# Kernel tuning notes

Hardware: AMD Instinct MI355X
Metric: run time of the kernel (lower is better)

## Reference

```python
import jax, jax.numpy as jnp
import numpy as np

B, P, ENC, DEC, ATT, EMB, V, T = 128, 196, 2048, 512, 512, 512, 10000, 30


def setup_inputs() -> dict:
    key = jax.random.key(0)
    ks = jax.random.split(key, 16)

    def lin(k, o, i, s=0.02):
        k1, k2 = jax.random.split(k)
        return (jax.random.normal(k1, (o, i), jnp.float32) * s,
                jax.random.normal(k2, (o,), jnp.float32) * s)

    enc_out = jax.random.normal(ks[0], (B, P, ENC), jnp.float32)
    enc_caps = jax.random.randint(ks[1], (B, T), 0, V)
    len_caps = jax.random.randint(ks[2], (B, 1), 2, T + 1)  # lengths in [2, T]

    W_enc_att, b_enc_att = lin(ks[3], ATT, ENC)
    W_dec_att, b_dec_att = lin(ks[4], ATT, DEC)
    W_att, b_att = lin(ks[5], 1, ATT)
    W_init_h, b_init_h = lin(ks[6], DEC, ENC)
    W_init_c, b_init_c = lin(ks[7], DEC, ENC)
    W_ih, b_ih = lin(ks[8], 4 * DEC, EMB + ENC)
    W_hh, b_hh = lin(ks[9], 4 * DEC, DEC)
    W_fbeta, b_fbeta = lin(ks[10], ENC, DEC)
    emb = jax.random.uniform(ks[11], (V, EMB), jnp.float32, -0.1, 0.1)
    W_fc = jax.random.uniform(ks[12], (V, DEC), jnp.float32, -0.1, 0.1)
    b_fc = jnp.zeros((V,), jnp.float32)

    return dict(enc_out=enc_out, enc_caps=enc_caps, len_caps=len_caps, emb=emb,
                W_enc_att=W_enc_att, b_enc_att=b_enc_att,
                W_dec_att=W_dec_att, b_dec_att=b_dec_att,
                W_att=W_att, b_att=b_att,
                W_init_h=W_init_h, b_init_h=b_init_h,
                W_init_c=W_init_c, b_init_c=b_init_c,
                W_ih=W_ih, b_ih=b_ih, W_hh=W_hh, b_hh=b_hh,
                W_fbeta=W_fbeta, b_fbeta=b_fbeta,
                W_fc=W_fc, b_fc=b_fc)


def _forward(enc_out, enc_caps, len_caps, emb,
             W_enc_att, b_enc_att, W_dec_att, b_dec_att, W_att, b_att,
             W_init_h, b_init_h, W_init_c, b_init_c,
             W_ih, b_ih, W_hh, b_hh, W_fbeta, b_fbeta, W_fc, b_fc):
    lens = len_caps[:, 0]
    order = jnp.argsort(-lens)  # sort descending by caption length
    lens = lens[order]
    caps = enc_caps[order]
    enc = enc_out[order]  # [B,P,ENC]
    len_dec = lens - 1
    Tm = caps.shape[1] - 1  # static upper bound on decode steps; masked per row

    embeds = emb[caps[:, :Tm]]  # [B,Tm,EMB]
    mu = enc.mean(axis=1)
    h = mu @ W_init_h.T + b_init_h
    c = mu @ W_init_c.T + b_init_c
    att_enc = enc @ W_enc_att.T + b_enc_att  # [B,P,ATT], invariant over t

    def step(carry, inp):
        h, c = carry
        t, emb_t = inp
        att_dec = h @ W_dec_att.T + b_dec_att  # [B,ATT]
        e = (jax.nn.relu(att_enc + att_dec[:, None, :]) @ W_att.T + b_att)[..., 0]  # [B,P]
        alpha = jax.nn.softmax(e, axis=1)
        weighted = jnp.einsum('bpd,bp->bd', enc, alpha)  # [B,ENC]
        gate = jax.nn.sigmoid(h @ W_fbeta.T + b_fbeta)
        x = jnp.concatenate([emb_t, weighted * gate], axis=1)  # [B,EMB+ENC]
        gates = x @ W_ih.T + b_ih + h @ W_hh.T + b_hh
        i, f, g, o = jnp.split(gates, 4, axis=1)  # torch LSTMCell gate order
        c_new = jax.nn.sigmoid(f) * c + jax.nn.sigmoid(i) * jnp.tanh(g)
        h_new = jax.nn.sigmoid(o) * jnp.tanh(c_new)
        preds = h_new @ W_fc.T + b_fc  # dropout is identity at eval
        m = (t < len_dec).astype(h.dtype)[:, None]  # shrinking-batch mask
        h = m * h_new + (1 - m) * h
        c = m * c_new + (1 - m) * c
        return (h, c), (preds * m, alpha * m)

    ts = jnp.arange(Tm)
    (_, _), (preds, alphas) = jax.lax.scan(step, (h, c), (ts, jnp.swapaxes(embeds, 0, 1)))
    predictions = jnp.swapaxes(preds, 0, 1)  # [B,Tm,V]
    alphas = jnp.swapaxes(alphas, 0, 1)      # [B,Tm,P]
    return caps, len_dec, predictions, alphas, order


def reference(enc_out, enc_caps, len_caps, emb,
              W_enc_att, b_enc_att, W_dec_att, b_dec_att, W_att, b_att,
              W_init_h, b_init_h, W_init_c, b_init_c,
              W_ih, b_ih, W_hh, b_hh, W_fbeta, b_fbeta, W_fc, b_fc):
    return _forward(enc_out, enc_caps, len_caps, emb,
                    W_enc_att, b_enc_att, W_dec_att, b_dec_att, W_att, b_att,
                    W_init_h, b_init_h, W_init_c, b_init_c,
                    W_ih, b_ih, W_hh, b_hh, W_fbeta, b_fbeta, W_fc, b_fc)
```

## Files before the change

### kernel.cpp

```cpp
#include <hip/hip_runtime.h>
#include <hip/hip_bf16.h>
#include <math.h>

#define NB   128
#define NP   196
#define DENC 2048
#define DDEC 512
#define NV   10000
#define NT   30
#define NTM  29

typedef __attribute__((ext_vector_type(8))) short short8;
typedef __attribute__((ext_vector_type(4))) float f32x4;

__device__ __forceinline__ float sigmoidf_(float x) { return 1.f / (1.f + __expf(-x)); }
__device__ __forceinline__ unsigned short f2bf(float x) {
    unsigned int u = __float_as_uint(x);
    u += 0x7fffu + ((u >> 16) & 1u);
    return (unsigned short)(u >> 16);
}
__device__ __forceinline__ float bf2f(unsigned short h) {
    return __uint_as_float(((unsigned int)h) << 16);
}

__global__ void sort_kernel(const int* __restrict__ len_caps,
                            const int* __restrict__ enc_caps,
                            float* __restrict__ out_caps,
                            float* __restrict__ out_lendec,
                            float* __restrict__ out_order,
                            int* __restrict__ order_ws,
                            int* __restrict__ nt_ws,
                            int* __restrict__ caps_ws) {
    __shared__ int lens[NB];
    int i = threadIdx.x;
    lens[i] = len_caps[i];
    __syncthreads();
    int li = lens[i];
    int r = 0;
    for (int j = 0; j < NB; ++j) {
        int lj = lens[j];
        if (lj > li || (lj == li && j < i)) r++;
    }
    order_ws[r]   = i;
    out_order[r]  = (float)i;
    out_lendec[r] = (float)(li - 1);
    for (int k = 0; k < NT; ++k) {
        int cv = enc_caps[i * NT + k];
        caps_ws[r * NT + k]  = cv;
        out_caps[r * NT + k] = (float)cv;
    }
    if (i < NTM) {
        int cnt = 0;
        for (int j = 0; j < NB; ++j) cnt += (lens[j] - 1 > i) ? 1 : 0;
        nt_ws[i] = cnt;
    }
}

__global__ void rowmap_kernel(const int* __restrict__ order, int* __restrict__ rowmap) {
    int m = blockIdx.x * 256 + threadIdx.x;
    rowmap[m] = order[m / NP] * NP + (m % NP);
}

__global__ void mu_kernel(const float* __restrict__ enc,
                          const int* __restrict__ order,
                          float* __restrict__ mu) {
    int b = blockIdx.x;
    int d = blockIdx.y * 256 + threadIdx.x;
    const float* eb = enc + (long)order[b] * NP * DENC;
    float s = 0.f;
    for (int p = 0; p < NP; ++p) s += eb[(long)p * DENC + d];
    mu[(long)b * DENC + d] = s * (1.f / (float)NP);
}

__global__ void fill_zero4(float4* __restrict__ p, int n4) {
    int i = blockIdx.x * 256 + threadIdx.x;
    if (i < n4) p[i] = make_float4(0.f, 0.f, 0.f, 0.f);
}

__global__ void conv_bf(const float* __restrict__ s, unsigned short* __restrict__ d, int n) {
    int i = blockIdx.x * 256 + threadIdx.x;
    if (i < n) d[i] = f2bf(s[i]);
}

__global__ void kconcat_ihh(const float* __restrict__ W_ih, const float* __restrict__ W_hh,
                            unsigned short* __restrict__ dst) {
    int n = blockIdx.y;
    int k = blockIdx.x * 256 + threadIdx.x;
    float v = (k < 2560) ? W_ih[(long)n * 2560 + k] : W_hh[(long)n * 512 + (k - 2560)];
    dst[(long)n * 3072 + k] = f2bf(v);
}

__global__ void bias_add2(const float* __restrict__ a, const float* __restrict__ b,
                          float* __restrict__ d, int n) {
    int i = blockIdx.x * 256 + threadIdx.x;
    if (i < n) d[i] = a[i] + b[i];
}

__global__ __launch_bounds__(256) void gemm_mfma(
    const float* __restrict__ A, long lda, const int* __restrict__ rowmap,
    const unsigned short* __restrict__ W, long ldw,
    const float* __restrict__ bias0, const float* __restrict__ bias1, int split,
    float* __restrict__ out0, long ld0, float* __restrict__ out1, long ld1,
    unsigned short* __restrict__ outbf,
    int act0, int act1, int M, int N, int K,
    const int* __restrict__ nt, int t, long zstride, int abf) {
    __shared__ __align__(16) unsigned short As[64 * 32];
    __shared__ __align__(16) unsigned short Bs[128 * 32];
    const int limit = nt ? nt[t] : M;

    int bx = blockIdx.x, by = blockIdx.y;
    if (!nt) {
        int nwg = gridDim.x * gridDim.y;
        int lin = by * gridDim.x + bx;
        int q = nwg >> 3, r = nwg & 7;
        int xcd = lin & 7, i = lin >> 3;
        int sw = (xcd < r ? xcd * (q + 1) : r * (q + 1) + (xcd - r) * q) + i;
        bx = sw % gridDim.x;
        by = sw / gridDim.x;
    }

    const int m0 = by * 64;
    if (m0 >= limit) return;
    const int n0 = bx * 128;
    const int tid = threadIdx.x;
    const int kz = blockIdx.z * K;

    const int arow = tid >> 2, akc = tid & 3;
    const int aws = (akc ^ ((arow >> 1) & 3)) * 8;
    const int brow = tid >> 1, bkc = (tid & 1) * 2;
    const int bss = (brow >> 1) & 3;
    const int bws0 = (bkc ^ bss) * 8;
    const int bws1 = ((bkc + 1) ^ bss) * 8;

    long aRowG = m0 + arow;
    if (rowmap) aRowG = rowmap[aRowG];
    const float* aptrf = nullptr;
    const unsigned short* aptrh = nullptr;
    if (abf) aptrh = (const unsigned short*)A + aRowG * lda + akc * 8 + kz;
    else     aptrf = A + aRowG * lda + akc * 8 + kz;
    const int gnw = n0 + brow;
    const bool wvalid = gnw < N;
    const unsigned short* wptr = W + (long)(wvalid ? gnw : 0) * ldw + bkc * 8 + kz;

    if (blockIdx.z) out0 += (long)blockIdx.z * zstride;

    const int lane = tid & 63, wv = tid >> 6;
    const int wm = wv & 1, wn = wv >> 1;
    const int fcol = lane & 15, quad = lane >> 4;
    const int sx = (fcol >> 1) & 3;
    const unsigned short* aFp = As + ((wm * 32 + fcol) * 32 + ((quad ^ sx) * 8));
    const unsigned short* bFp = Bs + ((wn * 64 + fcol) * 32 + ((quad ^ sx) * 8));

    f32x4 acc[2][4];
#pragma unroll
    for (int i = 0; i < 2; ++i)
#pragma unroll
        for (int j = 0; j < 4; ++j) acc[i][j] = (f32x4){0.f, 0.f, 0.f, 0.f};

    for (int k0 = 0; k0 < K; k0 += 32) {
        short8 ap;
        if (abf) {
            ap = *(const short8*)(aptrh);
            aptrh += 32;
        } else {
            float4 x0 = *(const float4*)(aptrf);
            float4 x1 = *(const float4*)(aptrf + 4);
            aptrf += 32;
            ap[0] = (short)f2bf(x0.x); ap[1] = (short)f2bf(x0.y);
            ap[2] = (short)f2bf(x0.z); ap[3] = (short)f2bf(x0.w);
            ap[4] = (short)f2bf(x1.x); ap[5] = (short)f2bf(x1.y);
            ap[6] = (short)f2bf(x1.z); ap[7] = (short)f2bf(x1.w);
        }
        int4 w0 = make_int4(0, 0, 0, 0), w1 = w0;
        if (wvalid) {
            w0 = *(const int4*)(wptr);
            w1 = *(const int4*)(wptr + 8);
        }
        wptr += 32;
        __syncthreads();
        *(short8*)(As + (arow * 32 + aws)) = ap;
        *(int4*)(Bs + (brow * 32 + bws0)) = w0;
        *(int4*)(Bs + (brow * 32 + bws1)) = w1;
        __syncthreads();
        short8 a0 = *(const short8*)(aFp);
        short8 a1 = *(const short8*)(aFp + 512);
#pragma unroll
        for (int ns = 0; ns < 4; ++ns) {
            short8 bn = *(const short8*)(bFp + ns * 512);
            acc[0][ns] = __builtin_amdgcn_mfma_f32_16x16x32_bf16(a0, bn, acc[0][ns], 0, 0, 0);
            acc[1][ns] = __builtin_amdgcn_mfma_f32_16x16x32_bf16(a1, bn, acc[1][ns], 0, 0, 0);
        }
    }

#pragma unroll
    for (int ms = 0; ms < 2; ++ms) {
        int gmb = m0 + wm * 32 + ms * 16 + quad * 4;
#pragma unroll
        for (int ns = 0; ns < 4; ++ns) {
            int gn = n0 + wn * 64 + ns * 16 + fcol;
            if (gn >= N) continue;
            int seg = (gn >= split);
            float bv = seg ? (bias1 ? bias1[gn - split] : 0.f)
                           : (bias0 ? bias0[gn] : 0.f);
            int act = seg ? act1 : act0;
#pragma unroll
            for (int r = 0; r < 4; ++r) {
                int gm = gmb + r;
                if (gm >= limit) continue;
                float v = acc[ms][ns][r] + bv;
                if (act == 1) v = sigmoidf_(v);
                if (outbf && !seg) outbf[(long)gm * ld0 + gn] = f2bf(v);
                else if (!seg) out0[(long)gm * ld0 + gn] = v;
                else out1[(long)gm * ld1 + (gn - split)] = v;
            }
        }
    }
}

__global__ __launch_bounds__(256) void alpha_kernel(
    const unsigned short* __restrict__ att_enc,
    const float* __restrict__ adg,
    const float* __restrict__ W_att, const float* __restrict__ b_att,
    const float* __restrict__ emb, const int* __restrict__ caps,
    const unsigned short* __restrict__ h_bf,
    const int* __restrict__ nt,
    float* __restrict__ al_g,
    float* __restrict__ out_alpha,
    unsigned short* __restrict__ xh, int t) {
    int b = blockIdx.x;
    if (b >= nt[t]) return;
    int tid = threadIdx.x, lane = tid & 63, wid = tid >> 6;
    __shared__ float es[NP];
    __shared__ float stats[2];

    const float* adp = adg + (long)b * 2560 + lane * 8;
    float4 ad0 = *(const float4*)(adp);
    float4 ad1 = *(const float4*)(adp + 4);
    const float* wap = W_att + lane * 8;
    float4 wa0 = *(const float4*)(wap);
    float4 wa1 = *(const float4*)(wap + 4);
    float ad[8] = {ad0.x, ad0.y, ad0.z, ad0.w, ad1.x, ad1.y, ad1.z, ad1.w};
    float wa[8] = {wa0.x, wa0.y, wa0.z, wa0.w, wa1.x, wa1.y, wa1.z, wa1.w};
    float batt = b_att[0];

    for (int p = wid; p < NP; p += 4) {
        const unsigned short* row = att_enc + ((long)b * NP + p) * 512 + lane * 8;
        int4 rv = *(const int4*)row;
        const unsigned short* us = (const unsigned short*)&rv;
        float s = 0.f;
#pragma unroll
        for (int j = 0; j < 8; ++j) {
            float v = bf2f(us[j]) + ad[j];
            v = v > 0.f ? v : 0.f;
            s += v * wa[j];
        }
#pragma unroll
        for (int o = 32; o; o >>= 1) s += __shfl_xor(s, o, 64);
        if (lane == 0) es[p] = s + batt;
    }
    __syncthreads();
    if (wid == 0) {
        float v[4], mx = -1e30f;
#pragma unroll
        for (int i = 0; i < 4; ++i) {
            int p = lane + 64 * i;
            v[i] = (p < NP) ? es[p] : -1e30f;
            mx = fmaxf(mx, v[i]);
        }
#pragma unroll
        for (int o = 32; o; o >>= 1) mx = fmaxf(mx, __shfl_xor(mx, o, 64));
        float s = 0.f;
#pragma unroll
        for (int i = 0; i < 4; ++i) {
            int p = lane + 64 * i;
            if (p < NP) s += __expf(v[i] - mx);
        }
#pragma unroll
        for (int o = 32; o; o >>= 1) s += __shfl_xor(s, o, 64);
        if (lane == 0) { stats[0] = mx; stats[1] = 1.f / s; }
    }
    __syncthreads();
    float mm = stats[0], inv = stats[1];
    if (tid < NP) {
        float a = __expf(es[tid] - mm) * inv;
        al_g[(long)b * NP + tid] = a;
        out_alpha[((long)b * NTM + t) * NP + tid] = a;
    }
    int cap = caps[b * NT + t];
    float2 ev = *(const float2*)(emb + (long)cap * 512 + tid * 2);
    unsigned int pk = (unsigned int)f2bf(ev.x) | ((unsigned int)f2bf(ev.y) << 16);
    *(unsigned int*)(xh + (long)b * 3072 + tid * 2) = pk;
    unsigned int hv = *(const unsigned int*)(h_bf + (long)b * DDEC + tid * 2);
    *(unsigned int*)(xh + (long)b * 3072 + 2560 + tid * 2) = hv;
}

__global__ __launch_bounds__(256) void wx_kernel(
    const float* __restrict__ al_g,
    const float* __restrict__ adg,
    const float* __restrict__ enc, const int* __restrict__ order,
    const int* __restrict__ nt,
    unsigned short* __restrict__ xh, int t) {
    int b = blockIdx.x;
    if (b >= nt[t]) return;
    int d = blockIdx.y * 256 + threadIdx.x;
    __shared__ float al[NP];
    if (threadIdx.x < NP) al[threadIdx.x] = al_g[(long)b * NP + threadIdx.x];
    __syncthreads();
    const float* eb = enc + ((long)order[b] * NP) * DENC + d;
    float acc = 0.f;
#pragma unroll 4
    for (int p = 0; p < NP; ++p) acc += al[p] * eb[(long)p * DENC];
    float gate = adg[(long)b * 2560 + 512 + d];
    xh[(long)b * 3072 + 512 + d] = f2bf(acc * gate);
}

__global__ void lstm_kernel(const float* __restrict__ gp,
                            const float* __restrict__ bihh,
                            float* __restrict__ c,
                            unsigned short* __restrict__ h_bf,
                            const int* __restrict__ nt, int t) {
    int b = blockIdx.y;
    if (b >= nt[t]) return;
    int d = blockIdx.x * 256 + threadIdx.x;
    const long S = (long)NB * 2048;
    const float* g = gp + ((long)b << 11);
    float ig = sigmoidf_(g[d]        + g[S + d]        + g[2*S + d]        + bihh[d]);
    float fg = sigmoidf_(g[512 + d]  + g[S + 512 + d]  + g[2*S + 512 + d]  + bihh[512 + d]);
    float gg = tanhf(    g[1024 + d] + g[S + 1024 + d] + g[2*S + 1024 + d] + bihh[1024 + d]);
    float og = sigmoidf_(g[1536 + d] + g[S + 1536 + d] + g[2*S + 1536 + d] + bihh[1536 + d]);
    long idx = (long)b * DDEC + d;
    float cn = fg * c[idx] + ig * gg;
    c[idx] = cn;
    h_bf[idx] = f2bf(og * tanhf(cn));
}

extern "C" void kernel_launch(void* const* d_in, const int* in_sizes, int n_in,
                              void* d_out, int out_size, void* d_ws, size_t ws_size,
                              hipStream_t stream) {
    const float* enc_out   = (const float*)d_in[0];
    const int*   enc_caps  = (const int*)d_in[1];
    const int*   len_caps  = (const int*)d_in[2];
    const float* emb       = (const float*)d_in[3];
    const float* W_enc_att = (const float*)d_in[4];
    const float* b_enc_att = (const float*)d_in[5];
    const float* W_dec_att = (const float*)d_in[6];
    const float* b_dec_att = (const float*)d_in[7];
    const float* W_att     = (const float*)d_in[8];
    const float* b_att     = (const float*)d_in[9];
    const float* W_init_h  = (const float*)d_in[10];
    const float* b_init_h  = (const float*)d_in[11];
    const float* W_init_c  = (const float*)d_in[12];
    const float* b_init_c  = (const float*)d_in[13];
    const float* W_ih      = (const float*)d_in[14];
    const float* b_ih      = (const float*)d_in[15];
    const float* W_hh      = (const float*)d_in[16];
    const float* b_hh      = (const float*)d_in[17];
    const float* W_fbeta   = (const float*)d_in[18];
    const float* b_fbeta   = (const float*)d_in[19];
    const float* W_fc      = (const float*)d_in[20];
    const float* b_fc      = (const float*)d_in[21];

    float* out        = (float*)d_out;
    float* out_caps   = out;
    float* out_lendec = out + 3840;
    float* out_pred   = out + 3968;
    float* out_alpha  = out + 3968 + 37120000;
    float* out_order  = out + 3968 + 37120000 + 727552;

    char*  wsb = (char*)d_ws;
    size_t off = 0;
    auto alloc = [&](size_t bytes) -> void* {
        void* p = wsb + off;
        off += (bytes + 255) & ~(size_t)255;
        return p;
    };
    int*   order_ws = (int*)alloc(NB * 4);
    int*   nt_ws    = (int*)alloc(NTM * 4);
    int*   caps_ws  = (int*)alloc(NB * NT * 4);
    int*   rowmap   = (int*)alloc((size_t)NB * NP * 4);
    float* mu       = (float*)alloc((size_t)NB * DENC * 4);
    float* c        = (float*)alloc((size_t)NB * DDEC * 4);
    float* adg      = (float*)alloc((size_t)NB * 2560 * 4);
    float* al_g     = (float*)alloc((size_t)NB * NP * 4);
    float* gates    = (float*)alloc((size_t)3 * NB * 2048 * 4);
    unsigned short* h_bf = (unsigned short*)alloc((size_t)NB * DDEC * 2);
    unsigned short* xh   = (unsigned short*)alloc((size_t)NB * 3072 * 2);
    unsigned short* att_enc_bf = (unsigned short*)alloc((size_t)NB * NP * 512 * 2);
    unsigned short* Wq_enc  = (unsigned short*)alloc((size_t)512 * 2048 * 2);
    unsigned short* Wq_init = (unsigned short*)alloc((size_t)1024 * 2048 * 2);
    unsigned short* Wq_adg  = (unsigned short*)alloc((size_t)2560 * 512 * 2);
    unsigned short* Wq_ihh  = (unsigned short*)alloc((size_t)2048 * 3072 * 2);
    unsigned short* Wq_fc   = (unsigned short*)alloc((size_t)NV * 512 * 2);
    float* bihh = (float*)alloc(2048 * 4);

    sort_kernel<<<1, NB, 0, stream>>>(len_caps, enc_caps, out_caps, out_lendec,
                                      out_order, order_ws, nt_ws, caps_ws);
    fill_zero4<<<36960, 256, 0, stream>>>((float4*)out_pred, 9461888);
    rowmap_kernel<<<98, 256, 0, stream>>>(order_ws, rowmap);
    mu_kernel<<<dim3(NB, DENC / 256), 256, 0, stream>>>(enc_out, order_ws, mu);

    conv_bf<<<(512 * 2048) / 256, 256, 0, stream>>>(W_enc_att, Wq_enc, 512 * 2048);
    conv_bf<<<(512 * 2048) / 256, 256, 0, stream>>>(W_init_h, Wq_init, 512 * 2048);
    conv_bf<<<(512 * 2048) / 256, 256, 0, stream>>>(W_init_c, Wq_init + (size_t)512 * 2048, 512 * 2048);
    conv_bf<<<(512 * 512) / 256, 256, 0, stream>>>(W_dec_att, Wq_adg, 512 * 512);
    conv_bf<<<(2048 * 512) / 256, 256, 0, stream>>>(W_fbeta, Wq_adg + (size_t)512 * 512, 2048 * 512);
    kconcat_ihh<<<dim3(12, 2048), 256, 0, stream>>>(W_ih, W_hh, Wq_ihh);
    conv_bf<<<(NV * 512) / 256, 256, 0, stream>>>(W_fc, Wq_fc, NV * 512);
    bias_add2<<<8, 256, 0, stream>>>(b_ih, b_hh, bihh, 2048);

    gemm_mfma<<<dim3(8, 2), 256, 0, stream>>>(
        mu, DENC, nullptr, Wq_init, DENC,
        b_init_h, b_init_c, 512,
        nullptr, DDEC, c, DDEC, h_bf, 0, 0,
        NB, 1024, DENC, nullptr, 0, 0, 0);

    gemm_mfma<<<dim3(4, 392), 256, 0, stream>>>(
        enc_out, DENC, rowmap, Wq_enc, DENC,
        b_enc_att, nullptr, 512,
        nullptr, 512, nullptr, 0, att_enc_bf, 0, 0,
        NB * NP, 512, DENC, nullptr, 0, 0, 0);

    for (int t = 0; t < NTM; ++t) {
        gemm_mfma<<<dim3(20, 2), 256, 0, stream>>>(
            (const float*)h_bf, DDEC, nullptr, Wq_adg, DDEC,
            b_dec_att, b_fbeta, 512,
            adg, 2560, adg + 512, 2560, nullptr, 0, 1,
            NB, 2560, DDEC, nt_ws, t, 0, 1);
        alpha_kernel<<<NB, 256, 0, stream>>>(
            att_enc_bf, adg, W_att, b_att, emb, caps_ws, h_bf, nt_ws,
            al_g, out_alpha, xh, t);
        wx_kernel<<<dim3(NB, 8), 256, 0, stream>>>(
            al_g, adg, enc_out, order_ws, nt_ws, xh, t);
        gemm_mfma<<<dim3(16, 2, 3), 256, 0, stream>>>(
            (const float*)xh, 3072, nullptr, Wq_ihh, 3072,
            nullptr, nullptr, 2048,
            gates, 2048, nullptr, 0, nullptr, 0, 0,
            NB, 2048, 1024, nt_ws, t, (long)NB * 2048, 1);
        lstm_kernel<<<dim3(2, NB), 256, 0, stream>>>(gates, bihh, c, h_bf, nt_ws, t);
        gemm_mfma<<<dim3(79, 2), 256, 0, stream>>>(
            (const float*)h_bf, DDEC, nullptr, Wq_fc, DDEC,
            b_fc, nullptr, NV,
            out_pred + (long)t * NV, (long)NTM * NV, nullptr, 0, nullptr, 0, 0,
            NB, NV, DDEC, nt_ws, t, 0, 1);
    }
}
```

Baseline: 4.086 ms.

## Pre-convert sorted encoder output to bf16 and double-buffer GEMM LDS tiles

Adds a kernel that gathers the encoder output in sorted order and converts it to bf16 once. The mean, attention-encoder GEMM and the per-step weighted-context kernel then read this half-size copy instead of the fp32 tensor, which cuts the bandwidth of the 29 repeated wx passes. The GEMM also gets double-buffered shared memory with a register prefetch, so global loads overlap the MFMA work and one barrier per k-step is removed. The cost is an extra 100 MB buffer and one conversion pass, and the mean and context sums are now taken over bf16-rounded inputs, which loses some precision.

```diff
diff --git a/kernel.cpp b/kernel.cpp
--- a/kernel.cpp
+++ b/kernel.cpp
@@ -61,15 +61,34 @@
     rowmap[m] = order[m / NP] * NP + (m % NP);
 }
 
-__global__ void mu_kernel(const float* __restrict__ enc,
-                          const int* __restrict__ order,
+__global__ void conv_enc_bf(const float* __restrict__ enc, const int* __restrict__ rowmap,
+                            unsigned short* __restrict__ dst) {
+    long m = blockIdx.x;
+    int d = threadIdx.x * 8;
+    const float* src = enc + (long)rowmap[m] * DENC + d;
+    float4 x0 = *(const float4*)(src);
+    float4 x1 = *(const float4*)(src + 4);
+    short8 v;
+    v[0] = (short)f2bf(x0.x); v[1] = (short)f2bf(x0.y);
+    v[2] = (short)f2bf(x0.z); v[3] = (short)f2bf(x0.w);
+    v[4] = (short)f2bf(x1.x); v[5] = (short)f2bf(x1.y);
+    v[6] = (short)f2bf(x1.z); v[7] = (short)f2bf(x1.w);
+    *(short8*)(dst + m * DENC + d) = v;
+}
+
+__global__ void mu_kernel(const unsigned short* __restrict__ enc_bfs,
                           float* __restrict__ mu) {
     int b = blockIdx.x;
-    int d = blockIdx.y * 256 + threadIdx.x;
-    const float* eb = enc + (long)order[b] * NP * DENC;
-    float s = 0.f;
-    for (int p = 0; p < NP; ++p) s += eb[(long)p * DENC + d];
-    mu[(long)b * DENC + d] = s * (1.f / (float)NP);
+    int d = (blockIdx.y * 256 + threadIdx.x) * 2;
+    const unsigned short* eb = enc_bfs + (long)b * NP * DENC + d;
+    float s0 = 0.f, s1 = 0.f;
+    for (int p = 0; p < NP; ++p) {
+        unsigned int pk = *(const unsigned int*)(eb + (long)p * DENC);
+        s0 += bf2f((unsigned short)(pk & 0xffffu));
+        s1 += bf2f((unsigned short)(pk >> 16));
+    }
+    mu[(long)b * DENC + d]     = s0 * (1.f / (float)NP);
+    mu[(long)b * DENC + d + 1] = s1 * (1.f / (float)NP);
 }
 
 __global__ void fill_zero4(float4* __restrict__ p, int n4) {
@@ -104,8 +123,8 @@
     unsigned short* __restrict__ outbf,
     int act0, int act1, int M, int N, int K,
     const int* __restrict__ nt, int t, long zstride, int abf) {
-    __shared__ __align__(16) unsigned short As[64 * 32];
-    __shared__ __align__(16) unsigned short Bs[128 * 32];
+    __shared__ __align__(16) unsigned short As[2][64 * 32];
+    __shared__ __align__(16) unsigned short Bs[2][128 * 32];
     const int limit = nt ? nt[t] : M;
 
     int bx = blockIdx.x, by = blockIdx.y;
@@ -148,8 +167,8 @@
     const int wm = wv & 1, wn = wv >> 1;
     const int fcol = lane & 15, quad = lane >> 4;
     const int sx = (fcol >> 1) & 3;
-    const unsigned short* aFp = As + ((wm * 32 + fcol) * 32 + ((quad ^ sx) * 8));
-    const unsigned short* bFp = Bs + ((wn * 64 + fcol) * 32 + ((quad ^ sx) * 8));
+    const int aOff = (wm * 32 + fcol) * 32 + ((quad ^ sx) * 8);
+    const int bOff = (wn * 64 + fcol) * 32 + ((quad ^ sx) * 8);
 
     f32x4 acc[2][4];
 #pragma unroll
@@ -157,39 +176,60 @@
 #pragma unroll
         for (int j = 0; j < 4; ++j) acc[i][j] = (f32x4){0.f, 0.f, 0.f, 0.f};
 
-    for (int k0 = 0; k0 < K; k0 += 32) {
-        short8 ap;
-        if (abf) {
-            ap = *(const short8*)(aptrh);
-            aptrh += 32;
-        } else {
-            float4 x0 = *(const float4*)(aptrf);
-            float4 x1 = *(const float4*)(aptrf + 4);
-            aptrf += 32;
-            ap[0] = (short)f2bf(x0.x); ap[1] = (short)f2bf(x0.y);
-            ap[2] = (short)f2bf(x0.z); ap[3] = (short)f2bf(x0.w);
-            ap[4] = (short)f2bf(x1.x); ap[5] = (short)f2bf(x1.y);
-            ap[6] = (short)f2bf(x1.z); ap[7] = (short)f2bf(x1.w);
+    const int nk = K >> 5;
+    float4 x0, x1;
+    short8 ap;
+    int4 w0 = make_int4(0, 0, 0, 0), w1 = w0;
+
+    auto gload = [&]() {
+        if (abf) { ap = *(const short8*)(aptrh); aptrh += 32; }
+        else { x0 = *(const float4*)(aptrf); x1 = *(const float4*)(aptrf + 4); aptrf += 32; }
+        if (wvalid) { w0 = *(const int4*)(wptr); w1 = *(const int4*)(wptr + 8); }
+        wptr += 32;
+    };
+    auto stage = [&](int buf) {
+        short8 av;
+        if (abf) av = ap;
+        else {
+            av[0] = (short)f2bf(x0.x); av[1] = (short)f2bf(x0.y);
+            av[2] = (short)f2bf(x0.z); av[3] = (short)f2bf(x0.w);
+            av[4] = (short)f2bf(x1.x); av[5] = (short)f2bf(x1.y);
+            av[6] = (short)f2bf(x1.z); av[7] = (short)f2bf(x1.w);
         }
-        int4 w0 = make_int4(0, 0, 0, 0), w1 = w0;
-        if (wvalid) {
-            w0 = *(const int4*)(wptr);
-            w1 = *(const int4*)(wptr + 8);
-        }
-        wptr += 32;
-        __syncthreads();
-        *(short8*)(As + (arow * 32 + aws)) = ap;
-        *(int4*)(Bs + (brow * 32 + bws0)) = w0;
-        *(int4*)(Bs + (brow * 32 + bws1)) = w1;
-        __syncthreads();
-        short8 a0 = *(const short8*)(aFp);
-        short8 a1 = *(const short8*)(aFp + 512);
-#pragma unroll
-        for (int ns = 0; ns < 4; ++ns) {
-            short8 bn = *(const short8*)(bFp + ns * 512);
-            acc[0][ns] = __builtin_amdgcn_mfma_f32_16x16x32_bf16(a0, bn, acc[0][ns], 0, 0, 0);
-            acc[1][ns] = __builtin_amdgcn_mfma_f32_16x16x32_bf16(a1, bn, acc[1][ns], 0, 0, 0);
-        }
+        *(short8*)(&As[buf][arow * 32 + aws]) = av;
+        *(int4*)(&Bs[buf][brow * 32 + bws0]) = w0;
+        *(int4*)(&Bs[buf][brow * 32 + bws1]) = w1;
+    };
+
+    gload();
+    stage(0);
+    asm volatile("s_waitcnt lgkmcnt(0)" ::: "memory");
+    __builtin_amdgcn_s_barrier();
+    __builtin_amdgcn_sched_barrier(0);
+    if (nk > 1) gload();
+
+    int cur = 0;
+    for (int kk = 0; kk < nk; ++kk) {
+        short8 a0 = *(const short8*)(&As[cur][aOff]);
+        short8 a1 = *(const short8*)(&As[cur][aOff + 512]);
+        short8 b0 = *(const short8*)(&Bs[cur][bOff]);
+        short8 b1 = *(const short8*)(&Bs[cur][bOff + 512]);
+        short8 b2 = *(const short8*)(&Bs[cur][bOff + 1024]);
+        short8 b3 = *(const short8*)(&Bs[cur][bOff + 1536]);
+        if (kk + 1 < nk) stage(cur ^ 1);
+        if (kk + 2 < nk) gload();
+        acc[0][0] = __builtin_amdgcn_mfma_f32_16x16x32_bf16(a0, b0, acc[0][0], 0, 0, 0);
+        acc[1][0] = __builtin_amdgcn_mfma_f32_16x16x32_bf16(a1, b0, acc[1][0], 0, 0, 0);
+        acc[0][1] = __builtin_amdgcn_mfma_f32_16x16x32_bf16(a0, b1, acc[0][1], 0, 0, 0);
+        acc[1][1] = __builtin_amdgcn_mfma_f32_16x16x32_bf16(a1, b1, acc[1][1], 0, 0, 0);
+        acc[0][2] = __builtin_amdgcn_mfma_f32_16x16x32_bf16(a0, b2, acc[0][2], 0, 0, 0);
+        acc[1][2] = __builtin_amdgcn_mfma_f32_16x16x32_bf16(a1, b2, acc[1][2], 0, 0, 0);
+        acc[0][3] = __builtin_amdgcn_mfma_f32_16x16x32_bf16(a0, b3, acc[0][3], 0, 0, 0);
+        acc[1][3] = __builtin_amdgcn_mfma_f32_16x16x32_bf16(a1, b3, acc[1][3], 0, 0, 0);
+        asm volatile("s_waitcnt lgkmcnt(0)" ::: "memory");
+        __builtin_amdgcn_s_barrier();
+        __builtin_amdgcn_sched_barrier(0);
+        cur ^= 1;
     }
 
 #pragma unroll
@@ -297,21 +337,28 @@
 __global__ __launch_bounds__(256) void wx_kernel(
     const float* __restrict__ al_g,
     const float* __restrict__ adg,
-    const float* __restrict__ enc, const int* __restrict__ order,
+    const unsigned short* __restrict__ enc_bfs,
     const int* __restrict__ nt,
     unsigned short* __restrict__ xh, int t) {
     int b = blockIdx.x;
     if (b >= nt[t]) return;
-    int d = blockIdx.y * 256 + threadIdx.x;
+    int d = (blockIdx.y * 256 + threadIdx.x) * 2;
     __shared__ float al[NP];
     if (threadIdx.x < NP) al[threadIdx.x] = al_g[(long)b * NP + threadIdx.x];
     __syncthreads();
-    const float* eb = enc + ((long)order[b] * NP) * DENC + d;
-    float acc = 0.f;
+    const unsigned short* eb = enc_bfs + (long)b * NP * DENC + d;
+    float a0 = 0.f, a1 = 0.f;
 #pragma unroll 4
-    for (int p = 0; p < NP; ++p) acc += al[p] * eb[(long)p * DENC];
-    float gate = adg[(long)b * 2560 + 512 + d];
-    xh[(long)b * 3072 + 512 + d] = f2bf(acc * gate);
+    for (int p = 0; p < NP; ++p) {
+        unsigned int pk = *(const unsigned int*)(eb + (long)p * DENC);
+        float w = al[p];
+        a0 += w * bf2f((unsigned short)(pk & 0xffffu));
+        a1 += w * bf2f((unsigned short)(pk >> 16));
+    }
+    float g0 = adg[(long)b * 2560 + 512 + d];
+    float g1 = adg[(long)b * 2560 + 512 + d + 1];
+    unsigned int o = (unsigned int)f2bf(a0 * g0) | ((unsigned int)f2bf(a1 * g1) << 16);
+    *(unsigned int*)(xh + (long)b * 3072 + 512 + d) = o;
 }
 
 __global__ void lstm_kernel(const float* __restrict__ gp,
@@ -385,6 +432,7 @@
     float* gates    = (float*)alloc((size_t)3 * NB * 2048 * 4);
     unsigned short* h_bf = (unsigned short*)alloc((size_t)NB * DDEC * 2);
     unsigned short* xh   = (unsigned short*)alloc((size_t)NB * 3072 * 2);
+    unsigned short* enc_bfs    = (unsigned short*)alloc((size_t)NB * NP * DENC * 2);
     unsigned short* att_enc_bf = (unsigned short*)alloc((size_t)NB * NP * 512 * 2);
     unsigned short* Wq_enc  = (unsigned short*)alloc((size_t)512 * 2048 * 2);
     unsigned short* Wq_init = (unsigned short*)alloc((size_t)1024 * 2048 * 2);
@@ -397,7 +445,8 @@
                                       out_order, order_ws, nt_ws, caps_ws);
     fill_zero4<<<36960, 256, 0, stream>>>((float4*)out_pred, 9461888);
     rowmap_kernel<<<98, 256, 0, stream>>>(order_ws, rowmap);
-    mu_kernel<<<dim3(NB, DENC / 256), 256, 0, stream>>>(enc_out, order_ws, mu);
+    conv_enc_bf<<<NB * NP, 256, 0, stream>>>(enc_out, rowmap, enc_bfs);
+    mu_kernel<<<dim3(NB, 4), 256, 0, stream>>>(enc_bfs, mu);
 
     conv_bf<<<(512 * 2048) / 256, 256, 0, stream>>>(W_enc_att, Wq_enc, 512 * 2048);
     conv_bf<<<(512 * 2048) / 256, 256, 0, stream>>>(W_init_h, Wq_init, 512 * 2048);
@@ -415,10 +464,10 @@
         NB, 1024, DENC, nullptr, 0, 0, 0);
 
     gemm_mfma<<<dim3(4, 392), 256, 0, stream>>>(
-        enc_out, DENC, rowmap, Wq_enc, DENC,
+        (const float*)enc_bfs, DENC, nullptr, Wq_enc, DENC,
         b_enc_att, nullptr, 512,
         nullptr, 512, nullptr, 0, att_enc_bf, 0, 0,
-        NB * NP, 512, DENC, nullptr, 0, 0, 0);
+        NB * NP, 512, DENC, nullptr, 0, 0, 1);
 
     for (int t = 0; t < NTM; ++t) {
         gemm_mfma<<<dim3(20, 2), 256, 0, stream>>>(
@@ -429,8 +478,8 @@
         alpha_kernel<<<NB, 256, 0, stream>>>(
             att_enc_bf, adg, W_att, b_att, emb, caps_ws, h_bf, nt_ws,
             al_g, out_alpha, xh, t);
-        wx_kernel<<<dim3(NB, 8), 256, 0, stream>>>(
-            al_g, adg, enc_out, order_ws, nt_ws, xh, t);
+        wx_kernel<<<dim3(NB, 4), 256, 0, stream>>>(
+            al_g, adg, enc_bfs, nt_ws, xh, t);
         gemm_mfma<<<dim3(16, 2, 3), 256, 0, stream>>>(
             (const float*)xh, 3072, nullptr, Wq_ihh, 3072,
             nullptr, nullptr, 2048,
```

After: 4.138 ms. No clear change (+1.3%).
